# Optimization experiments

Hardware: AMD Instinct MI355X
Metric: run time of the kernel (lower is better)

Reference implementation:

```python
import jax, jax.numpy as jnp
import numpy as np

# ---- constants mirroring the externally-set attributes of AttentionControl ----
B = 512            # batch_size
STATE = 512        # dim of recurrent core state `output`
S = 224            # mnist_size (image H == W)
SB = 16            # sensorBandwidth
DEPTH = 3
SCALING = 2
PIXEL_SCALING = 1.0
UNITS = 2          # 2-D glimpse location
HG = 128; HL = 128; G = 256
TSB = DEPTH * SB * SB                      # totalSensorBandwidth = 768
OFFSET = SB * SCALING ** (DEPTH - 1)       # 64: pad so all crops stay in-bounds


def hard_tanh(x):
    return jnp.clip(x, -1.0, 1.0)


def _dense_params(key, fan_in, fan_out):
    # keras RandomNormal(mean=0.1, stddev=0.05) kernel, zero bias
    return 0.1 + 0.05 * jax.random.normal(key, (fan_in, fan_out), jnp.float32), jnp.zeros((fan_out,), jnp.float32)


def setup_inputs() -> dict:
    key = jax.random.key(0)
    ks = jax.random.split(key, 8)
    W_loc, b_loc = _dense_params(ks[0], STATE, UNITS)      # h_location_out
    W_hg, b_hg = _dense_params(ks[1], TSB, HG)             # h_glimpse_layer
    W_hl, b_hl = _dense_params(ks[2], UNITS, HL)           # h_location_layer
    W_gs, b_gs = _dense_params(ks[3], HG, G)               # h_glimpse_layer_sum
    W_ls, b_ls = _dense_params(ks[4], HL, G)               # h_location_layer_sum
    return {
        "output": jax.random.normal(ks[5], (B, STATE), jnp.float32),
        "inputs": jax.random.uniform(ks[6], (B, S, S, 1), jnp.float32),
        "W_loc": W_loc, "b_loc": b_loc,
        "W_hg": W_hg, "b_hg": b_hg,
        "W_hl": W_hl, "b_hl": b_hl,
        "W_gs": W_gs, "b_gs": b_gs,
        "W_ls": W_ls, "b_ls": b_ls,
    }


def _extract_glimpses(inputs, loc_int):
    """inputs: [B,S,S,1]; loc_int: [B,2] int32 pixel locations.
    Returns [B, DEPTH, SB, SB] multi-scale glimpses."""
    img = inputs[..., 0]
    padded = jnp.pad(img, ((0, 0), (OFFSET, OFFSET), (OFFSET, OFFSET)))

    def per_sample(im, l):
        zooms = []
        for i in range(DEPTH):
            d = SB * SCALING ** i
            start = OFFSET + l - d // 2
            z = jax.lax.dynamic_slice(im, (start[0], start[1]), (d, d))
            if i > 0:
                z = jax.image.resize(z, (SB, SB), method="bilinear")
            zooms.append(z)
        return jnp.stack(zooms)  # [DEPTH, SB, SB]

    return jax.vmap(per_sample)(padded, loc_int)


def reference(output, inputs, W_loc, b_loc, W_hg, b_hg, W_hl, b_hl, W_gs, b_gs, W_ls, b_ls):
    # eval mode: tf.cond(training, noise, 0.0) -> 0.0
    mean_loc = hard_tanh(jax.lax.stop_gradient(output) @ W_loc + b_loc)  # [B, 2]
    sample_loc = hard_tanh(mean_loc)
    loc = sample_loc * PIXEL_SCALING
    # glimpseSensor
    loc_int = jnp.round((loc + 1.0) / 2.0 * S).astype(jnp.int32)
    glimpses = _extract_glimpses(inputs, loc_int).reshape(B, TSB)
    # Glimpse network fusion
    hg = jax.nn.relu(glimpses @ W_hg + b_hg)
    hl = jax.nn.relu(loc @ W_hl + b_hl)
    g = jax.nn.relu(hg @ W_gs + b_gs + hl @ W_ls + b_ls)  # [B, G]
    return g
```

## Files before the change

### kernel.cpp

```cpp
#include <hip/hip_runtime.h>
#include <math.h>

#define NB    512
#define STATE 512
#define IMS   224
#define TSB   768
#define HGN   128
#define GN    256
#define WPITCH 65

__device__ __forceinline__ void d1w(int o, float w[4]) {
    w[0] = 0.125f; w[1] = 0.375f; w[2] = 0.375f; w[3] = 0.125f;
    if (o == 0)  { w[0] = 0.f;      w[1] = 3.f/7.f; w[2] = 3.f/7.f; w[3] = 1.f/7.f; }
    if (o == 15) { w[0] = 1.f/7.f;  w[1] = 3.f/7.f; w[2] = 3.f/7.f; w[3] = 0.f; }
}
__device__ __forceinline__ void d2w(int o, float w[8]) {
    const float s = 1.f/32.f;
    w[0]=1*s; w[1]=3*s; w[2]=5*s; w[3]=7*s; w[4]=7*s; w[5]=5*s; w[6]=3*s; w[7]=1*s;
    if (o == 0)  { const float t=1.f/28.f; w[0]=0.f; w[1]=0.f; w[2]=5*t; w[3]=7*t; w[4]=7*t; w[5]=5*t; w[6]=3*t; w[7]=1*t; }
    if (o == 15) { const float t=1.f/28.f; w[0]=1*t; w[1]=3*t; w[2]=5*t; w[3]=7*t; w[4]=7*t; w[5]=5*t; w[6]=0.f; w[7]=0.f; }
}

__global__ __launch_bounds__(512) void fused_attn(
    const float* __restrict__ out_state,
    const float* __restrict__ img,
    const float* __restrict__ W_loc, const float* __restrict__ b_loc,
    const float* __restrict__ W_hg,  const float* __restrict__ b_hg,
    const float* __restrict__ W_hl,  const float* __restrict__ b_hl,
    const float* __restrict__ W_gs,  const float* __restrict__ b_gs,
    const float* __restrict__ W_ls,  const float* __restrict__ b_ls,
    float* __restrict__ out)
{
    __shared__ float win[2][64 * WPITCH];
    __shared__ float gl[2][TSB];
    __shared__ float s_hg[2][HGN];
    __shared__ float s_hl[2][HGN];
    __shared__ float part4[2][16][HGN];
    __shared__ float part6[2][8][GN];
    __shared__ float red[8][2];
    __shared__ float s_loc[2][2];
    __shared__ int   s_li[2][2];

    const int t  = threadIdx.x;
    const int b0 = blockIdx.x * 2;

    {
        int s = t >> 8, k = t & 255;
        const float* orow = out_state + (size_t)(b0 + s) * STATE;
        float x0 = orow[k], x1 = orow[k + 256];
        float a0 = x0 * W_loc[k*2]     + x1 * W_loc[(k+256)*2];
        float a1 = x0 * W_loc[k*2 + 1] + x1 * W_loc[(k+256)*2 + 1];
        for (int off = 32; off; off >>= 1) {
            a0 += __shfl_down(a0, off);
            a1 += __shfl_down(a1, off);
        }
        if ((t & 63) == 0) { red[t>>6][0] = a0; red[t>>6][1] = a1; }
    }
    __syncthreads();
    if ((t & 255) == 0) {
        int s = t >> 8;
        float l0 = red[4*s][0]+red[4*s+1][0]+red[4*s+2][0]+red[4*s+3][0] + b_loc[0];
        float l1 = red[4*s][1]+red[4*s+1][1]+red[4*s+2][1]+red[4*s+3][1] + b_loc[1];
        l0 = fminf(fmaxf(l0, -1.f), 1.f);
        l1 = fminf(fmaxf(l1, -1.f), 1.f);
        s_loc[s][0] = l0; s_loc[s][1] = l1;
        s_li[s][0] = (int)rintf((l0 + 1.f) * 0.5f * (float)IMS);
        s_li[s][1] = (int)rintf((l1 + 1.f) * 0.5f * (float)IMS);
    }
    __syncthreads();

    #pragma unroll
    for (int i = 0; i < 16; ++i) {
        int idx = t + i * 512;
        int s = idx >> 12, rem = idx & 4095;
        int r = rem >> 6, c = rem & 63;
        int rr = s_li[s][0] - 32 + r, cc = s_li[s][1] - 32 + c;
        float v = 0.f;
        if ((unsigned)rr < (unsigned)IMS && (unsigned)cc < (unsigned)IMS)
            v = img[(size_t)(b0 + s) * IMS * IMS + rr * IMS + cc];
        win[s][r * WPITCH + c] = v;
    }
    __syncthreads();

    {
        int s = t >> 8, p = t & 255, r = p >> 4, c = p & 15;
        const float* w = win[s];
        gl[s][p] = w[(24 + r) * WPITCH + (24 + c)];
        {
            float wr[4], wc[4];
            d1w(r, wr); d1w(c, wc);
            int jr0 = 16 + 2*r - 1, jc0 = 16 + 2*c - 1;
            float acc = 0.f;
            #pragma unroll
            for (int a = 0; a < 4; ++a) {
                float rowsum = 0.f;
                #pragma unroll
                for (int bb = 0; bb < 4; ++bb)
                    rowsum += wc[bb] * w[(jr0 + a) * WPITCH + (jc0 + bb)];
                acc += wr[a] * rowsum;
            }
            gl[s][256 + p] = acc;
        }
        {
            float wr[8], wc[8];
            d2w(r, wr); d2w(c, wc);
            int jr0 = 4*r - 2, jc0 = 4*c - 2;
            float acc = 0.f;
            #pragma unroll
            for (int a = 0; a < 8; ++a) {
                int jr = min(max(jr0 + a, 0), 63);
                float rowsum = 0.f;
                #pragma unroll
                for (int bb = 0; bb < 8; ++bb) {
                    int jc = min(max(jc0 + bb, 0), 63);
                    rowsum += wc[bb] * w[jr * WPITCH + jc];
                }
                acc += wr[a] * rowsum;
            }
            gl[s][512 + p] = acc;
        }
    }
    __syncthreads();

    {
        int cg = t & 31, q = t >> 5;
        const float* g0 = gl[0] + q * 48;
        const float* g1 = gl[1] + q * 48;
        const float* wp = W_hg + (size_t)(q * 48) * HGN + cg * 4;
        float4 acc0 = make_float4(0.f, 0.f, 0.f, 0.f);
        float4 acc1 = make_float4(0.f, 0.f, 0.f, 0.f);
        #pragma unroll 8
        for (int k = 0; k < 48; ++k) {
            float4 w4 = *(const float4*)(wp + (size_t)k * HGN);
            float a = g0[k], b = g1[k];
            acc0.x += a * w4.x; acc0.y += a * w4.y;
            acc0.z += a * w4.z; acc0.w += a * w4.w;
            acc1.x += b * w4.x; acc1.y += b * w4.y;
            acc1.z += b * w4.z; acc1.w += b * w4.w;
        }
        *(float4*)&part4[0][q][cg * 4] = acc0;
        *(float4*)&part4[1][q][cg * 4] = acc1;
    }
    __syncthreads();
    {
        int u = t & 255, s = u >> 7, col = u & 127;
        if (t < 256) {
            float a = b_hg[col];
            #pragma unroll
            for (int q = 0; q < 16; ++q) a += part4[s][q][col];
            s_hg[s][col] = fmaxf(a, 0.f);
        } else {
            float l0 = s_loc[s][0], l1 = s_loc[s][1];
            s_hl[s][col] = fmaxf(l0 * W_hl[col] + l1 * W_hl[HGN + col] + b_hl[col], 0.f);
        }
    }
    __syncthreads();

    {
        int cg = t & 63, q = t >> 6;
        const float* hg0 = s_hg[0] + q * 16;
        const float* hg1 = s_hg[1] + q * 16;
        const float* hl0 = s_hl[0] + q * 16;
        const float* hl1 = s_hl[1] + q * 16;
        const float* wgs = W_gs + (size_t)(q * 16) * GN + cg * 4;
        const float* wls = W_ls + (size_t)(q * 16) * GN + cg * 4;
        float4 acc0 = make_float4(0.f, 0.f, 0.f, 0.f);
        float4 acc1 = make_float4(0.f, 0.f, 0.f, 0.f);
        #pragma unroll 8
        for (int j = 0; j < 16; ++j) {
            float4 a4 = *(const float4*)(wgs + (size_t)j * GN);
            float4 b4 = *(const float4*)(wls + (size_t)j * GN);
            float hga = hg0[j], hgb = hg1[j];
            float hla = hl0[j], hlb = hl1[j];
            acc0.x += hga * a4.x + hla * b4.x;
            acc0.y += hga * a4.y + hla * b4.y;
            acc0.z += hga * a4.z + hla * b4.z;
            acc0.w += hga * a4.w + hla * b4.w;
            acc1.x += hgb * a4.x + hlb * b4.x;
            acc1.y += hgb * a4.y + hlb * b4.y;
            acc1.z += hgb * a4.z + hlb * b4.z;
            acc1.w += hgb * a4.w + hlb * b4.w;
        }
        *(float4*)&part6[0][q][cg * 4] = acc0;
        *(float4*)&part6[1][q][cg * 4] = acc1;
    }
    __syncthreads();
    {
        int s = t >> 8, n = t & 255;
        float a = b_gs[n] + b_ls[n];
        #pragma unroll
        for (int q = 0; q < 8; ++q) a += part6[s][q][n];
        out[(size_t)(b0 + s) * GN + n] = fmaxf(a, 0.f);
    }
}

extern "C" void kernel_launch(void* const* d_in, const int* in_sizes, int n_in,
                              void* d_out, int out_size, void* d_ws, size_t ws_size,
                              hipStream_t stream) {
    const float* out_state = (const float*)d_in[0];
    const float* img       = (const float*)d_in[1];
    const float* W_loc     = (const float*)d_in[2];
    const float* b_loc     = (const float*)d_in[3];
    const float* W_hg      = (const float*)d_in[4];
    const float* b_hg      = (const float*)d_in[5];
    const float* W_hl      = (const float*)d_in[6];
    const float* b_hl      = (const float*)d_in[7];
    const float* W_gs      = (const float*)d_in[8];
    const float* b_gs      = (const float*)d_in[9];
    const float* W_ls      = (const float*)d_in[10];
    const float* b_ls      = (const float*)d_in[11];
    float* out = (float*)d_out;

    hipLaunchKernelGGL(fused_attn, dim3(NB/2), dim3(512), 0, stream,
                       out_state, img, W_loc, b_loc, W_hg, b_hg,
                       W_hl, b_hl, W_gs, b_gs, W_ls, b_ls, out);
}
```

Measured before the change: 17.09 us.

## Process four samples per block and alias shared-memory buffers

Each block now handles four batch samples instead of two, which halves the grid to 128 blocks. The aim is to reuse each weight load from W_hg, W_gs and W_ls across four samples and cut global weight traffic. To fit four 64x65 windows in LDS, the window buffer is aliased with the partial-sum buffers in one manually laid-out byte array of about 83KB. The risk is that 128 blocks fill only about half of the MI355X's CUs, and the heavier LDS use per block lowers occupancy.

```diff
diff --git a/kernel.cpp b/kernel.cpp
--- a/kernel.cpp
+++ b/kernel.cpp
@@ -8,6 +8,18 @@
 #define HGN   128
 #define GN    256
 #define WPITCH 65
+#define SPB   4
+
+#define SM_WIN   0
+#define SM_P4    0
+#define SM_P6    32768
+#define SM_GL    66560
+#define SM_HG    78848
+#define SM_HL    80896
+#define SM_RED   82944
+#define SM_LOC   83008
+#define SM_LI    83040
+#define SM_TOTAL 83072
 
 __device__ __forceinline__ void d1w(int o, float w[4]) {
     w[0] = 0.125f; w[1] = 0.375f; w[2] = 0.375f; w[3] = 0.125f;
@@ -31,61 +43,69 @@
     const float* __restrict__ W_ls,  const float* __restrict__ b_ls,
     float* __restrict__ out)
 {
-    __shared__ float win[2][64 * WPITCH];
-    __shared__ float gl[2][TSB];
-    __shared__ float s_hg[2][HGN];
-    __shared__ float s_hl[2][HGN];
-    __shared__ float part4[2][16][HGN];
-    __shared__ float part6[2][8][GN];
-    __shared__ float red[8][2];
-    __shared__ float s_loc[2][2];
-    __shared__ int   s_li[2][2];
+    __shared__ __align__(16) char smem[SM_TOTAL];
+    float* win   = (float*)(smem + SM_WIN);
+    float* part4 = (float*)(smem + SM_P4);
+    float* part6 = (float*)(smem + SM_P6);
+    float* gl    = (float*)(smem + SM_GL);
+    float* s_hg  = (float*)(smem + SM_HG);
+    float* s_hl  = (float*)(smem + SM_HL);
+    float* red   = (float*)(smem + SM_RED);
+    float* s_loc = (float*)(smem + SM_LOC);
+    int*   s_li  = (int*)(smem + SM_LI);
 
     const int t  = threadIdx.x;
-    const int b0 = blockIdx.x * 2;
-
-    {
-        int s = t >> 8, k = t & 255;
+    const int b0 = blockIdx.x * SPB;
+
+    {
+        int s = t >> 7, k = t & 127;
         const float* orow = out_state + (size_t)(b0 + s) * STATE;
-        float x0 = orow[k], x1 = orow[k + 256];
-        float a0 = x0 * W_loc[k*2]     + x1 * W_loc[(k+256)*2];
-        float a1 = x0 * W_loc[k*2 + 1] + x1 * W_loc[(k+256)*2 + 1];
+        float a0 = 0.f, a1 = 0.f;
+        #pragma unroll
+        for (int i = 0; i < 4; ++i) {
+            float x = orow[k + i * 128];
+            a0 += x * W_loc[(k + i*128) * 2];
+            a1 += x * W_loc[(k + i*128) * 2 + 1];
+        }
         for (int off = 32; off; off >>= 1) {
             a0 += __shfl_down(a0, off);
             a1 += __shfl_down(a1, off);
         }
-        if ((t & 63) == 0) { red[t>>6][0] = a0; red[t>>6][1] = a1; }
-    }
-    __syncthreads();
-    if ((t & 255) == 0) {
-        int s = t >> 8;
-        float l0 = red[4*s][0]+red[4*s+1][0]+red[4*s+2][0]+red[4*s+3][0] + b_loc[0];
-        float l1 = red[4*s][1]+red[4*s+1][1]+red[4*s+2][1]+red[4*s+3][1] + b_loc[1];
+        if ((t & 63) == 0) { red[(t>>6)*2] = a0; red[(t>>6)*2 + 1] = a1; }
+    }
+    __syncthreads();
+    if ((t & 127) == 0) {
+        int s = t >> 7;
+        float l0 = red[4*s]     + red[4*s + 2] + b_loc[0];
+        float l1 = red[4*s + 1] + red[4*s + 3] + b_loc[1];
         l0 = fminf(fmaxf(l0, -1.f), 1.f);
         l1 = fminf(fmaxf(l1, -1.f), 1.f);
-        s_loc[s][0] = l0; s_loc[s][1] = l1;
-        s_li[s][0] = (int)rintf((l0 + 1.f) * 0.5f * (float)IMS);
-        s_li[s][1] = (int)rintf((l1 + 1.f) * 0.5f * (float)IMS);
+        s_loc[s*2] = l0; s_loc[s*2 + 1] = l1;
+        s_li[s*2]     = (int)rintf((l0 + 1.f) * 0.5f * (float)IMS);
+        s_li[s*2 + 1] = (int)rintf((l1 + 1.f) * 0.5f * (float)IMS);
     }
     __syncthreads();
 
     #pragma unroll
-    for (int i = 0; i < 16; ++i) {
+    for (int i = 0; i < 32; ++i) {
         int idx = t + i * 512;
         int s = idx >> 12, rem = idx & 4095;
         int r = rem >> 6, c = rem & 63;
-        int rr = s_li[s][0] - 32 + r, cc = s_li[s][1] - 32 + c;
+        int rr = s_li[s*2] - 32 + r, cc = s_li[s*2 + 1] - 32 + c;
         float v = 0.f;
         if ((unsigned)rr < (unsigned)IMS && (unsigned)cc < (unsigned)IMS)
             v = img[(size_t)(b0 + s) * IMS * IMS + rr * IMS + cc];
-        win[s][r * WPITCH + c] = v;
-    }
-    __syncthreads();
-
-    {
-        int s = t >> 8, p = t & 255, r = p >> 4, c = p & 15;
-        const float* w = win[s];
-        gl[s][p] = w[(24 + r) * WPITCH + (24 + c)];
+        win[s * (64*WPITCH) + r * WPITCH + c] = v;
+    }
+    __syncthreads();
+
+    #pragma unroll
+    for (int ii = 0; ii < 2; ++ii) {
+        int idx = t + ii * 512;
+        int s = idx >> 8, p = idx & 255, r = p >> 4, c = p & 15;
+        const float* w = win + s * (64*WPITCH);
+        float* glp = gl + s * TSB;
+        glp[p] = w[(24 + r) * WPITCH + (24 + c)];
         {
             float wr[4], wc[4];
             d1w(r, wr); d1w(c, wc);
@@ -99,7 +119,7 @@
                     rowsum += wc[bb] * w[(jr0 + a) * WPITCH + (jc0 + bb)];
                 acc += wr[a] * rowsum;
             }
-            gl[s][256 + p] = acc;
+            glp[256 + p] = acc;
         }
         {
             float wr[8], wc[8];
@@ -117,80 +137,87 @@
                 }
                 acc += wr[a] * rowsum;
             }
-            gl[s][512 + p] = acc;
+            glp[512 + p] = acc;
         }
     }
     __syncthreads();
 
     {
         int cg = t & 31, q = t >> 5;
-        const float* g0 = gl[0] + q * 48;
-        const float* g1 = gl[1] + q * 48;
+        const float* g0 = gl + 0*TSB + q * 48;
+        const float* g1 = gl + 1*TSB + q * 48;
+        const float* g2 = gl + 2*TSB + q * 48;
+        const float* g3 = gl + 3*TSB + q * 48;
         const float* wp = W_hg + (size_t)(q * 48) * HGN + cg * 4;
-        float4 acc0 = make_float4(0.f, 0.f, 0.f, 0.f);
-        float4 acc1 = make_float4(0.f, 0.f, 0.f, 0.f);
+        float4 acc0 = make_float4(0.f,0.f,0.f,0.f);
+        float4 acc1 = acc0, acc2 = acc0, acc3 = acc0;
         #pragma unroll 8
         for (int k = 0; k < 48; ++k) {
             float4 w4 = *(const float4*)(wp + (size_t)k * HGN);
-            float a = g0[k], b = g1[k];
-            acc0.x += a * w4.x; acc0.y += a * w4.y;
-            acc0.z += a * w4.z; acc0.w += a * w4.w;
-            acc1.x += b * w4.x; acc1.y += b * w4.y;
-            acc1.z += b * w4.z; acc1.w += b * w4.w;
-        }
-        *(float4*)&part4[0][q][cg * 4] = acc0;
-        *(float4*)&part4[1][q][cg * 4] = acc1;
-    }
-    __syncthreads();
-    {
-        int u = t & 255, s = u >> 7, col = u & 127;
-        if (t < 256) {
-            float a = b_hg[col];
-            #pragma unroll
-            for (int q = 0; q < 16; ++q) a += part4[s][q][col];
-            s_hg[s][col] = fmaxf(a, 0.f);
-        } else {
-            float l0 = s_loc[s][0], l1 = s_loc[s][1];
-            s_hl[s][col] = fmaxf(l0 * W_hl[col] + l1 * W_hl[HGN + col] + b_hl[col], 0.f);
-        }
+            float a = g0[k], b = g1[k], c = g2[k], d = g3[k];
+            acc0.x += a*w4.x; acc0.y += a*w4.y; acc0.z += a*w4.z; acc0.w += a*w4.w;
+            acc1.x += b*w4.x; acc1.y += b*w4.y; acc1.z += b*w4.z; acc1.w += b*w4.w;
+            acc2.x += c*w4.x; acc2.y += c*w4.y; acc2.z += c*w4.z; acc2.w += c*w4.w;
+            acc3.x += d*w4.x; acc3.y += d*w4.y; acc3.z += d*w4.z; acc3.w += d*w4.w;
+        }
+        *(float4*)&part4[(0*16 + q)*HGN + cg*4] = acc0;
+        *(float4*)&part4[(1*16 + q)*HGN + cg*4] = acc1;
+        *(float4*)&part4[(2*16 + q)*HGN + cg*4] = acc2;
+        *(float4*)&part4[(3*16 + q)*HGN + cg*4] = acc3;
+    }
+    __syncthreads();
+
+    {
+        int s = t >> 7, col = t & 127;
+        float a = b_hg[col];
+        #pragma unroll
+        for (int q = 0; q < 16; ++q) a += part4[(s*16 + q)*HGN + col];
+        s_hg[s*HGN + col] = fmaxf(a, 0.f);
+        float l0 = s_loc[s*2], l1 = s_loc[s*2 + 1];
+        s_hl[s*HGN + col] = fmaxf(l0 * W_hl[col] + l1 * W_hl[HGN + col] + b_hl[col], 0.f);
     }
     __syncthreads();
 
     {
         int cg = t & 63, q = t >> 6;
-        const float* hg0 = s_hg[0] + q * 16;
-        const float* hg1 = s_hg[1] + q * 16;
-        const float* hl0 = s_hl[0] + q * 16;
-        const float* hl1 = s_hl[1] + q * 16;
         const float* wgs = W_gs + (size_t)(q * 16) * GN + cg * 4;
         const float* wls = W_ls + (size_t)(q * 16) * GN + cg * 4;
-        float4 acc0 = make_float4(0.f, 0.f, 0.f, 0.f);
-        float4 acc1 = make_float4(0.f, 0.f, 0.f, 0.f);
-        #pragma unroll 8
+        float4 acc0 = make_float4(0.f,0.f,0.f,0.f);
+        float4 acc1 = acc0, acc2 = acc0, acc3 = acc0;
+        #pragma unroll 4
         for (int j = 0; j < 16; ++j) {
             float4 a4 = *(const float4*)(wgs + (size_t)j * GN);
             float4 b4 = *(const float4*)(wls + (size_t)j * GN);
-            float hga = hg0[j], hgb = hg1[j];
-            float hla = hl0[j], hlb = hl1[j];
-            acc0.x += hga * a4.x + hla * b4.x;
-            acc0.y += hga * a4.y + hla * b4.y;
-            acc0.z += hga * a4.z + hla * b4.z;
-            acc0.w += hga * a4.w + hla * b4.w;
-            acc1.x += hgb * a4.x + hlb * b4.x;
-            acc1.y += hgb * a4.y + hlb * b4.y;
-            acc1.z += hgb * a4.z + hlb * b4.z;
-            acc1.w += hgb * a4.w + hlb * b4.w;
-        }
-        *(float4*)&part6[0][q][cg * 4] = acc0;
-        *(float4*)&part6[1][q][cg * 4] = acc1;
-    }
-    __syncthreads();
-    {
-        int s = t >> 8, n = t & 255;
-        float a = b_gs[n] + b_ls[n];
+            int jj = q * 16 + j;
+            float hg0 = s_hg[0*HGN + jj], hl0 = s_hl[0*HGN + jj];
+            float hg1 = s_hg[1*HGN + jj], hl1 = s_hl[1*HGN + jj];
+            float hg2 = s_hg[2*HGN + jj], hl2 = s_hl[2*HGN + jj];
+            float hg3 = s_hg[3*HGN + jj], hl3 = s_hl[3*HGN + jj];
+            acc0.x += hg0*a4.x + hl0*b4.x; acc0.y += hg0*a4.y + hl0*b4.y;
+            acc0.z += hg0*a4.z + hl0*b4.z; acc0.w += hg0*a4.w + hl0*b4.w;
+            acc1.x += hg1*a4.x + hl1*b4.x; acc1.y += hg1*a4.y + hl1*b4.y;
+            acc1.z += hg1*a4.z + hl1*b4.z; acc1.w += hg1*a4.w + hl1*b4.w;
+            acc2.x += hg2*a4.x + hl2*b4.x; acc2.y += hg2*a4.y + hl2*b4.y;
+            acc2.z += hg2*a4.z + hl2*b4.z; acc2.w += hg2*a4.w + hl2*b4.w;
+            acc3.x += hg3*a4.x + hl3*b4.x; acc3.y += hg3*a4.y + hl3*b4.y;
+            acc3.z += hg3*a4.z + hl3*b4.z; acc3.w += hg3*a4.w + hl3*b4.w;
+        }
+        *(float4*)&part6[(0*8 + q)*GN + cg*4] = acc0;
+        *(float4*)&part6[(1*8 + q)*GN + cg*4] = acc1;
+        *(float4*)&part6[(2*8 + q)*GN + cg*4] = acc2;
+        *(float4*)&part6[(3*8 + q)*GN + cg*4] = acc3;
+    }
+    __syncthreads();
+    {
+        int n = t & 255, s0 = t >> 8;
         #pragma unroll
-        for (int q = 0; q < 8; ++q) a += part6[s][q][n];
-        out[(size_t)(b0 + s) * GN + n] = fmaxf(a, 0.f);
+        for (int sl = 0; sl < 2; ++sl) {
+            int s = s0 + sl * 2;
+            float a = b_gs[n] + b_ls[n];
+            #pragma unroll
+            for (int q = 0; q < 8; ++q) a += part6[(s*8 + q)*GN + n];
+            out[(size_t)(b0 + s) * GN + n] = fmaxf(a, 0.f);
+        }
     }
 }
 
@@ -211,7 +238,7 @@
     const float* b_ls      = (const float*)d_in[11];
     float* out = (float*)d_out;
 
-    hipLaunchKernelGGL(fused_attn, dim3(NB/2), dim3(512), 0, stream,
+    hipLaunchKernelGGL(fused_attn, dim3(NB/SPB), dim3(512), 0, stream,
                        out_state, img, W_loc, b_loc, W_hg, b_hg,
                        W_hl, b_hl, W_gs, b_gs, W_ls, b_ls, out);
 }
```

Measured after the change: 20.52 us. +20.1%, slower.

## Split fused kernel into glimpse, hidden-layer and output kernels with 4-sample batching

Applied to the files above, without the earlier changes.

The single fused kernel is split into three launches that pass intermediates through workspace memory: glimpse extraction, the W_hg layer, and the final G layer. The two GEMV kernels now handle 4 samples per block instead of 2, so each weight load is reused across more samples and weight traffic drops. The cost is two extra kernel launches and global round-trips for the glimpses and hidden activations, which at this small total runtime may outweigh the lower weight traffic.

```diff
diff --git a/kernel.cpp b/kernel.cpp
--- a/kernel.cpp
+++ b/kernel.cpp
@@ -21,22 +21,18 @@
     if (o == 15) { const float t=1.f/28.f; w[0]=1*t; w[1]=3*t; w[2]=5*t; w[3]=7*t; w[4]=7*t; w[5]=5*t; w[6]=0.f; w[7]=0.f; }
 }
 
-__global__ __launch_bounds__(512) void fused_attn(
+#define FMA4(acc, sc, w4) \
+    acc.x += (sc) * (w4).x; acc.y += (sc) * (w4).y; \
+    acc.z += (sc) * (w4).z; acc.w += (sc) * (w4).w;
+
+__global__ __launch_bounds__(512) void k1_glimpse(
     const float* __restrict__ out_state,
     const float* __restrict__ img,
     const float* __restrict__ W_loc, const float* __restrict__ b_loc,
-    const float* __restrict__ W_hg,  const float* __restrict__ b_hg,
-    const float* __restrict__ W_hl,  const float* __restrict__ b_hl,
-    const float* __restrict__ W_gs,  const float* __restrict__ b_gs,
-    const float* __restrict__ W_ls,  const float* __restrict__ b_ls,
-    float* __restrict__ out)
+    float* __restrict__ gl_g,
+    float* __restrict__ loc_g)
 {
     __shared__ float win[2][64 * WPITCH];
-    __shared__ float gl[2][TSB];
-    __shared__ float s_hg[2][HGN];
-    __shared__ float s_hl[2][HGN];
-    __shared__ float part4[2][16][HGN];
-    __shared__ float part6[2][8][GN];
     __shared__ float red[8][2];
     __shared__ float s_loc[2][2];
     __shared__ int   s_li[2][2];
@@ -66,6 +62,8 @@
         s_loc[s][0] = l0; s_loc[s][1] = l1;
         s_li[s][0] = (int)rintf((l0 + 1.f) * 0.5f * (float)IMS);
         s_li[s][1] = (int)rintf((l1 + 1.f) * 0.5f * (float)IMS);
+        loc_g[(b0 + s)*2 + 0] = l0;
+        loc_g[(b0 + s)*2 + 1] = l1;
     }
     __syncthreads();
 
@@ -85,7 +83,8 @@
     {
         int s = t >> 8, p = t & 255, r = p >> 4, c = p & 15;
         const float* w = win[s];
-        gl[s][p] = w[(24 + r) * WPITCH + (24 + c)];
+        float* glb = gl_g + (size_t)(b0 + s) * TSB;
+        glb[p] = w[(24 + r) * WPITCH + (24 + c)];
         {
             float wr[4], wc[4];
             d1w(r, wr); d1w(c, wc);
@@ -99,7 +98,7 @@
                     rowsum += wc[bb] * w[(jr0 + a) * WPITCH + (jc0 + bb)];
                 acc += wr[a] * rowsum;
             }
-            gl[s][256 + p] = acc;
+            glb[256 + p] = acc;
         }
         {
             float wr[8], wc[8];
@@ -117,80 +116,118 @@
                 }
                 acc += wr[a] * rowsum;
             }
-            gl[s][512 + p] = acc;
-        }
+            glb[512 + p] = acc;
+        }
+    }
+}
+
+__global__ __launch_bounds__(512) void k2_hg(
+    const float* __restrict__ gl_g,
+    const float* __restrict__ W_hg,
+    const float* __restrict__ b_hg,
+    float* __restrict__ hg_g)
+{
+    __shared__ float gls[4][TSB];
+    __shared__ float part[16][4][HGN];
+    const int t  = threadIdx.x;
+    const int b0 = blockIdx.x * 4;
+
+    {
+        const float4* src = (const float4*)(gl_g + (size_t)b0 * TSB);
+        float4* dst = (float4*)&gls[0][0];
+        dst[t] = src[t];
+        if (t < 256) dst[512 + t] = src[512 + t];
     }
     __syncthreads();
 
     {
         int cg = t & 31, q = t >> 5;
-        const float* g0 = gl[0] + q * 48;
-        const float* g1 = gl[1] + q * 48;
+        const float* g0 = gls[0] + q * 48;
+        const float* g1 = gls[1] + q * 48;
+        const float* g2 = gls[2] + q * 48;
+        const float* g3 = gls[3] + q * 48;
         const float* wp = W_hg + (size_t)(q * 48) * HGN + cg * 4;
-        float4 acc0 = make_float4(0.f, 0.f, 0.f, 0.f);
-        float4 acc1 = make_float4(0.f, 0.f, 0.f, 0.f);
+        float4 acc0 = make_float4(0.f,0.f,0.f,0.f);
+        float4 acc1 = acc0, acc2 = acc0, acc3 = acc0;
         #pragma unroll 8
         for (int k = 0; k < 48; ++k) {
             float4 w4 = *(const float4*)(wp + (size_t)k * HGN);
-            float a = g0[k], b = g1[k];
-            acc0.x += a * w4.x; acc0.y += a * w4.y;
-            acc0.z += a * w4.z; acc0.w += a * w4.w;
-            acc1.x += b * w4.x; acc1.y += b * w4.y;
-            acc1.z += b * w4.z; acc1.w += b * w4.w;
-        }
-        *(float4*)&part4[0][q][cg * 4] = acc0;
-        *(float4*)&part4[1][q][cg * 4] = acc1;
-    }
-    __syncthreads();
-    {
-        int u = t & 255, s = u >> 7, col = u & 127;
-        if (t < 256) {
-            float a = b_hg[col];
-            #pragma unroll
-            for (int q = 0; q < 16; ++q) a += part4[s][q][col];
-            s_hg[s][col] = fmaxf(a, 0.f);
-        } else {
-            float l0 = s_loc[s][0], l1 = s_loc[s][1];
-            s_hl[s][col] = fmaxf(l0 * W_hl[col] + l1 * W_hl[HGN + col] + b_hl[col], 0.f);
-        }
+            FMA4(acc0, g0[k], w4);
+            FMA4(acc1, g1[k], w4);
+            FMA4(acc2, g2[k], w4);
+            FMA4(acc3, g3[k], w4);
+        }
+        *(float4*)&part[q][0][cg * 4] = acc0;
+        *(float4*)&part[q][1][cg * 4] = acc1;
+        *(float4*)&part[q][2][cg * 4] = acc2;
+        *(float4*)&part[q][3][cg * 4] = acc3;
+    }
+    __syncthreads();
+
+    {
+        int s = t >> 7, col = t & 127;
+        float a = b_hg[col];
+        #pragma unroll
+        for (int q = 0; q < 16; ++q) a += part[q][s][col];
+        hg_g[(size_t)(b0 + s) * HGN + col] = fmaxf(a, 0.f);
+    }
+}
+
+__global__ __launch_bounds__(512) void k3_g(
+    const float* __restrict__ hg_g,
+    const float* __restrict__ loc_g,
+    const float* __restrict__ W_hl,  const float* __restrict__ b_hl,
+    const float* __restrict__ W_gs,  const float* __restrict__ b_gs,
+    const float* __restrict__ W_ls,  const float* __restrict__ b_ls,
+    float* __restrict__ out)
+{
+    __shared__ float s_hg[4][HGN];
+    __shared__ float s_hl[4][HGN];
+    __shared__ float part[8][4][GN];
+    const int t  = threadIdx.x;
+    const int b0 = blockIdx.x * 4;
+
+    {
+        int s = t >> 7, col = t & 127;
+        s_hg[s][col] = hg_g[(size_t)(b0 + s) * HGN + col];
+        float l0 = loc_g[(b0 + s)*2], l1 = loc_g[(b0 + s)*2 + 1];
+        s_hl[s][col] = fmaxf(l0 * W_hl[col] + l1 * W_hl[HGN + col] + b_hl[col], 0.f);
     }
     __syncthreads();
 
     {
         int cg = t & 63, q = t >> 6;
-        const float* hg0 = s_hg[0] + q * 16;
-        const float* hg1 = s_hg[1] + q * 16;
-        const float* hl0 = s_hl[0] + q * 16;
-        const float* hl1 = s_hl[1] + q * 16;
         const float* wgs = W_gs + (size_t)(q * 16) * GN + cg * 4;
         const float* wls = W_ls + (size_t)(q * 16) * GN + cg * 4;
-        float4 acc0 = make_float4(0.f, 0.f, 0.f, 0.f);
-        float4 acc1 = make_float4(0.f, 0.f, 0.f, 0.f);
-        #pragma unroll 8
+        float4 acc0 = make_float4(0.f,0.f,0.f,0.f);
+        float4 acc1 = acc0, acc2 = acc0, acc3 = acc0;
+        #pragma unroll 4
         for (int j = 0; j < 16; ++j) {
             float4 a4 = *(const float4*)(wgs + (size_t)j * GN);
             float4 b4 = *(const float4*)(wls + (size_t)j * GN);
-            float hga = hg0[j], hgb = hg1[j];
-            float hla = hl0[j], hlb = hl1[j];
-            acc0.x += hga * a4.x + hla * b4.x;
-            acc0.y += hga * a4.y + hla * b4.y;
-            acc0.z += hga * a4.z + hla * b4.z;
-            acc0.w += hga * a4.w + hla * b4.w;
-            acc1.x += hgb * a4.x + hlb * b4.x;
-            acc1.y += hgb * a4.y + hlb * b4.y;
-            acc1.z += hgb * a4.z + hlb * b4.z;
-            acc1.w += hgb * a4.w + hlb * b4.w;
-        }
-        *(float4*)&part6[0][q][cg * 4] = acc0;
-        *(float4*)&part6[1][q][cg * 4] = acc1;
-    }
-    __syncthreads();
-    {
-        int s = t >> 8, n = t & 255;
-        float a = b_gs[n] + b_ls[n];
+            int jj = q * 16 + j;
+            FMA4(acc0, s_hg[0][jj], a4); FMA4(acc0, s_hl[0][jj], b4);
+            FMA4(acc1, s_hg[1][jj], a4); FMA4(acc1, s_hl[1][jj], b4);
+            FMA4(acc2, s_hg[2][jj], a4); FMA4(acc2, s_hl[2][jj], b4);
+            FMA4(acc3, s_hg[3][jj], a4); FMA4(acc3, s_hl[3][jj], b4);
+        }
+        *(float4*)&part[q][0][cg * 4] = acc0;
+        *(float4*)&part[q][1][cg * 4] = acc1;
+        *(float4*)&part[q][2][cg * 4] = acc2;
+        *(float4*)&part[q][3][cg * 4] = acc3;
+    }
+    __syncthreads();
+
+    {
+        int n = t & 255, s0 = t >> 8;
         #pragma unroll
-        for (int q = 0; q < 8; ++q) a += part6[s][q][n];
-        out[(size_t)(b0 + s) * GN + n] = fmaxf(a, 0.f);
+        for (int sl = 0; sl < 2; ++sl) {
+            int s = s0 + sl * 2;
+            float a = b_gs[n] + b_ls[n];
+            #pragma unroll
+            for (int q = 0; q < 8; ++q) a += part[q][s][n];
+            out[(size_t)(b0 + s) * GN + n] = fmaxf(a, 0.f);
+        }
     }
 }
 
@@ -211,7 +248,15 @@
     const float* b_ls      = (const float*)d_in[11];
     float* out = (float*)d_out;
 
-    hipLaunchKernelGGL(fused_attn, dim3(NB/2), dim3(512), 0, stream,
-                       out_state, img, W_loc, b_loc, W_hg, b_hg,
-                       W_hl, b_hl, W_gs, b_gs, W_ls, b_ls, out);
-}
+    char* ws = (char*)d_ws;
+    float* gl_g  = (float*)(ws);
+    float* loc_g = (float*)(ws + (size_t)NB*TSB*4);
+    float* hg_g  = (float*)(ws + (size_t)NB*TSB*4 + 4096);
+
+    hipLaunchKernelGGL(k1_glimpse, dim3(NB/2), dim3(512), 0, stream,
+                       out_state, img, W_loc, b_loc, gl_g, loc_g);
+    hipLaunchKernelGGL(k2_hg, dim3(NB/4), dim3(512), 0, stream,
+                       gl_g, W_hg, b_hg, hg_g);
+    hipLaunchKernelGGL(k3_g, dim3(NB/4), dim3(512), 0, stream,
+                       hg_g, loc_g, W_hl, b_hl, W_gs, b_gs, W_ls, b_ls, out);
+}
```

Result: slower. 20.50 us (+19.9%).
